# Kernel optimization log

Hardware: AMD Instinct MI355X
Metric: run time of the kernel (lower is better)

The kernel has to match this reference:

```python
import jax, jax.numpy as jnp
import numpy as np

NUM_HEADS = 16

def setup_inputs() -> dict:
    key = jax.random.key(0)
    k1, k2, k3, k4 = jax.random.split(key, 4)
    B, S, D = 4, 4096, 2048
    scale = 1.0 / np.sqrt(D)
    return {
        "x": jax.random.normal(k1, (B, S, D), dtype=jnp.float32),
        "W_q": jax.random.normal(k2, (D, D), dtype=jnp.float32) * scale,
        "W_kv": jax.random.normal(k3, (D, D), dtype=jnp.float32) * scale,
        "W_o": jax.random.normal(k4, (D, D), dtype=jnp.float32) * scale,
    }

def _l2_normalize_complex(z):
    # torch.norm(z, dim=-1, keepdim=True) for complex: sqrt(sum |z|^2)
    n = jnp.sqrt(jnp.sum(jnp.abs(z) ** 2, axis=-1, keepdims=True))
    return z / n

def reference(x, W_q, W_kv, W_o):
    B, S, D = x.shape
    H = NUM_HEADS
    hd = D // H
    # Linear (no bias), torch convention: x @ W.T
    q = (x @ W_q.T).reshape(B, S, H, hd)
    kv = (x @ W_kv.T).reshape(B, S, H, hd)
    # HRR binding: FFT along head dim
    qf = jnp.fft.fft(q, axis=-1)
    kvf = jnp.fft.fft(kv, axis=-1)
    qf = _l2_normalize_complex(qf)
    kvf = _l2_normalize_complex(kvf)
    # causal=True: cumulative sum of bound key-values over sequence
    kvf = jnp.cumsum(kvf, axis=1)
    qv = qf * kvf
    values_hat = jnp.fft.ifft(qv, axis=-1).real.astype(x.dtype)
    values_hat = values_hat.reshape(B, S, D)
    return values_hat @ W_o.T
```

## Files before the change

kernel.cpp:

```cpp
#include <hip/hip_runtime.h>
#include <hip/hip_bf16.h>


typedef unsigned short u16;
typedef unsigned int u32;
typedef __attribute__((ext_vector_type(8))) short short8;
typedef __attribute__((ext_vector_type(4))) float f32x4;

__device__ __forceinline__ float bf2f(u16 u) {
  u32 x = ((u32)u) << 16;
  float f; __builtin_memcpy(&f, &x, 4); return f;
}
__device__ __forceinline__ u16 f2bf(float f) {
  __hip_bfloat16 h = __float2bfloat16(f);
  u16 u; __builtin_memcpy(&u, &h, 2); return u;
}
__device__ __forceinline__ u32 pack2(float a, float b) {
  return (u32)f2bf(a) | ((u32)f2bf(b) << 16);
}

#define GLD16(gp, lp)                                                        \
  __builtin_amdgcn_global_load_lds(                                          \
      (const __attribute__((address_space(1))) void*)(gp),                   \
      (__attribute__((address_space(3))) void*)(lp), 16, 0, 0)

__device__ __forceinline__ unsigned ldsoff(const void* p) {
  return (unsigned)(size_t)(const __attribute__((address_space(3))) char*)p;
}

#define DSR(dst, ad, im)                                                     \
  asm volatile("ds_read_b128 %0, %1 offset:%c2"                              \
               : "=v"(dst) : "v"(ad), "i"(im))

#define MM2(ACCE, X0, X1, Y0, Y1)                                            \
  ACCE = __builtin_amdgcn_mfma_f32_16x16x32_bf16(X0, Y0, ACCE, 0, 0, 0);     \
  ACCE = __builtin_amdgcn_mfma_f32_16x16x32_bf16(X1, Y1, ACCE, 0, 0, 0)

template <int EPI>
__global__ __launch_bounds__(512, 2) void gemm256(
    const u16* __restrict__ A, const u16* __restrict__ B, void* __restrict__ C,
    int N, int K) {
  __shared__ alignas(1024) char smem[131072];
  const int NT = K >> 6;
  const int ntn = N >> 8;
  const int nwg = gridDim.x;
  int wg = blockIdx.x;
  wg = (wg & 7) * (nwg >> 3) + (wg >> 3);
  const int bm = wg / ntn, bn = wg % ntn;
  const long rowBase = (long)bm << 8, colBase = (long)bn << 8;

  const int tid = threadIdx.x;
  const int w = tid >> 6, lane = tid & 63;
  const int quad = lane >> 4, l16 = lane & 15;
  const int wm = w >> 2, wn = w & 3;

  const int grow = w * 8 + (lane >> 3);
  const int gcol = ((lane & 7) * 8) ^ ((lane >> 4) << 4);
  const long voff = (long)grow * K + gcol;
  const u16* Abase = A + rowBase * (long)K;
  const u16* Bbase = B + colBase * (long)K;
  char* ldsA = smem;
  char* ldsB = smem + 65536;

#define STG_A(v, h)                                                          \
  do {                                                                       \
    char* d_ = ldsA + (((v)&1) << 15) + ((h) << 14) + (w << 10);             \
    GLD16(Abase + ((h) * 128L) * K + (long)(v) * 64 + voff, d_);             \
    GLD16(Abase + ((h) * 128L + 64) * K + (long)(v) * 64 + voff, d_ + 8192); \
  } while (0)
#define STG_B(v, h)                                                          \
  do {                                                                       \
    char* d_ = ldsB + (((v)&1) << 15) + ((h) << 14) + (w << 10);             \
    GLD16(Bbase + ((h) * 128L) * K + (long)(v) * 64 + voff, d_);             \
    GLD16(Bbase + ((h) * 128L + 64) * K + (long)(v) * 64 + voff, d_ + 8192); \
  } while (0)

  const int cb0 = (quad << 4) ^ (((l16 >> 1) & 3) << 5);
  const unsigned bA0 = ldsoff(ldsA + (wm * 128 + l16) * 128) + cb0;
  const unsigned bA1 = bA0 ^ 64;
  const unsigned bB0 = ldsoff(ldsB + (wn * 64 + l16) * 128) + cb0;
  const unsigned bB1 = bB0 ^ 64;

  short8 aL[8], aH[8], bl[4], bh[4];
  f32x4 acc[8][4] = {};

  STG_A(0, 0); STG_A(0, 1); STG_B(0, 0); STG_B(0, 1);
  STG_B(1, 0); STG_B(1, 1);
  asm volatile("s_waitcnt vmcnt(4)");
  __builtin_amdgcn_s_barrier();

#define CLUSTER(BODY)                                                        \
  __builtin_amdgcn_sched_barrier(0);                                         \
  __builtin_amdgcn_s_setprio(1);                                             \
  BODY                                                                       \
  __builtin_amdgcn_s_setprio(0);                                             \
  __builtin_amdgcn_sched_barrier(0)

#define Q3P_BODY                                                             \
  _Pragma("unroll") for (int i = 0; i < 4; i++)                              \
    _Pragma("unroll") for (int j = 0; j < 2; j++) {                          \
      MM2(acc[i+4][j+2], aH[2*i], aH[2*i+1], bh[2*j], bh[2*j+1]);            \
    }
#define Q0_BODY                                                              \
  _Pragma("unroll") for (int i = 0; i < 4; i++)                              \
    _Pragma("unroll") for (int j = 0; j < 2; j++) {                          \
      MM2(acc[i][j], aL[2*i], aL[2*i+1], bl[2*j], bl[2*j+1]);                \
    }
#define Q1_BODY                                                              \
  _Pragma("unroll") for (int i = 0; i < 4; i++)                              \
    _Pragma("unroll") for (int j = 0; j < 2; j++) {                          \
      MM2(acc[i][j+2], aL[2*i], aL[2*i+1], bh[2*j], bh[2*j+1]);              \
    }
#define Q2_BODY                                                              \
  _Pragma("unroll") for (int i = 0; i < 4; i++)                              \
    _Pragma("unroll") for (int j = 0; j < 2; j++) {                          \
      MM2(acc[i+4][j], aH[2*i], aH[2*i+1], bl[2*j], bl[2*j+1]);              \
    }

#define RUN_TILE(uu, Q3P, SA_, SB_, WAITSTMT)                                \
  do {                                                                       \
    const unsigned bsel = ((uu) & 1) << 15;                                  \
    const unsigned aA0 = bA0 ^ bsel, aA1 = bA1 ^ bsel;                       \
    const unsigned aB0 = bB0 ^ bsel, aB1 = bB1 ^ bsel;                       \
                        \
    _Pragma("unroll") for (int i = 0; i < 4; i++) {                          \
      DSR(aL[2*i],   aA0, i * 2048);                                         \
      DSR(aL[2*i+1], aA1, i * 2048);                                         \
    }                                                                        \
    _Pragma("unroll") for (int j = 0; j < 2; j++) {                          \
      DSR(bl[2*j],   aB0, j * 2048);                                         \
      DSR(bl[2*j+1], aB1, j * 2048);                                         \
    }                                                                        \
    if (SA_) STG_A((uu) + 1, 0);                                             \
    __builtin_amdgcn_s_barrier();                                            \
    if (Q3P) { CLUSTER(Q3P_BODY); }                                          \
    __builtin_amdgcn_s_barrier();                                            \
      \
    _Pragma("unroll") for (int j = 0; j < 2; j++) {                          \
      DSR(bh[2*j],   aB0, (j + 2) * 2048);                                   \
      DSR(bh[2*j+1], aB1, (j + 2) * 2048);                                   \
    }                                                                        \
    if (SA_) STG_A((uu) + 1, 1);                                             \
    __builtin_amdgcn_s_barrier();                                            \
    asm volatile("s_waitcnt lgkmcnt(4)");                                    \
    CLUSTER(Q0_BODY);                                                        \
    __builtin_amdgcn_s_barrier();                                            \
         \
    _Pragma("unroll") for (int i = 0; i < 4; i++) {                          \
      DSR(aH[2*i],   aA0, (i + 4) * 2048);                                   \
      DSR(aH[2*i+1], aA1, (i + 4) * 2048);                                   \
    }                                                                        \
    if (SB_) STG_B((uu) + 2, 0);                                             \
    __builtin_amdgcn_s_barrier();                                            \
    asm volatile("s_waitcnt lgkmcnt(8)");                                    \
    CLUSTER(Q1_BODY);                                                        \
    __builtin_amdgcn_s_barrier();                                            \
        \
    if (SB_) STG_B((uu) + 2, 1);                                             \
    __builtin_amdgcn_s_barrier();                                            \
    asm volatile("s_waitcnt lgkmcnt(0)");                                    \
    CLUSTER(Q2_BODY);                                                        \
    WAITSTMT;                                                                \
    __builtin_amdgcn_s_barrier();                                            \
  } while (0)

  RUN_TILE(0, false, true, true, asm volatile("s_waitcnt vmcnt(4)"));
  for (int u = 1; u < NT - 2; ++u) {
    RUN_TILE(u, true, true, true, asm volatile("s_waitcnt vmcnt(4)"));
  }
  RUN_TILE(NT - 2, true, true, false, asm volatile("s_waitcnt vmcnt(0)"));
  RUN_TILE(NT - 1, true, false, false, (void)0);
  { Q3P_BODY }
#undef RUN_TILE
#undef Q3P_BODY
#undef Q0_BODY
#undef Q1_BODY
#undef Q2_BODY
#undef CLUSTER
#undef STG_A
#undef STG_B

  asm volatile("" ::: "memory");

  float scl[8][4];
#pragma unroll
  for (int i = 0; i < 8; i++)
#pragma unroll
    for (int r = 0; r < 4; r++) scl[i][r] = 1.0f;

  if (EPI == 2) {
    float* ssb = (float*)smem;
    __syncthreads();
#pragma unroll
    for (int i = 0; i < 8; i++)
#pragma unroll
      for (int r = 0; r < 4; r++) {
        float s = 0.f;
#pragma unroll
        for (int j = 0; j < 4; j++) { float v = acc[i][j][r]; s += v * v; }
        s += __shfl_xor(s, 1); s += __shfl_xor(s, 2);
        s += __shfl_xor(s, 4); s += __shfl_xor(s, 8);
        if (l16 == 0) ssb[((wm * 128 + i * 16 + quad * 4 + r) << 2) + wn] = s;
      }
    __syncthreads();
#pragma unroll
    for (int i = 0; i < 8; i++)
#pragma unroll
      for (int r = 0; r < 4; r++) {
        int row = wm * 128 + i * 16 + quad * 4 + r;
        float s = ssb[(row << 2) + (wn & 2)] + ssb[(row << 2) + (wn & 2) + 1];
        scl[i][r] = rsqrtf(128.0f * s);
      }
  }

#pragma unroll
  for (int i = 0; i < 8; i++) {
#pragma unroll
    for (int j = 0; j < 4; j++) {
      long row0 = rowBase + wm * 128 + i * 16 + quad * 4;
      long col = colBase + wn * 64 + j * 16 + l16;
#pragma unroll
      for (int r = 0; r < 4; r++) {
        float v = acc[i][j][r] * scl[i][r];
        long off = (row0 + r) * (long)N + col;
        if (EPI == 0) ((float*)C)[off] = v;
        else          ((u16*)C)[off] = f2bf(v);
      }
    }
  }
}

template <int EPI, bool FOLD>
__global__ __launch_bounds__(256, 2) void gemm_bt(
    const u16* __restrict__ A, const u16* __restrict__ B, void* __restrict__ C,
    int M, int N, int K, int lda) {
  const int ntiles = N >> 7;
  const int bid = blockIdx.x;
  const int bm = bid / ntiles, bn = bid % ntiles;
  const long rowBase = (long)bm * 128, colBase = (long)bn * 128;
  const long aOff = FOLD ? colBase : 0;
  const long bRowBase = FOLD ? 0 : colBase;

  __shared__ u16 As[128 * 32];
  __shared__ u16 Bs[128 * 32];
  __shared__ float ssbuf[128][2];

  const int tid = threadIdx.x;
  const int wave = tid >> 6, lane = tid & 63;
  const int quad = lane >> 4, l16 = lane & 15;
  const int waveRow = (wave >> 1) * 64, waveCol = (wave & 1) * 64;

  const int srow = lane >> 2, scol = (lane & 3) * 8;
  const u16* pa = A + (rowBase + wave * 32 + srow) * (long)lda + aOff + scol;
  const u16* pb = B + (bRowBase + wave * 32 + srow) * (long)K + scol;
  u16* lA0 = &As[(wave * 32) * 32];
  u16* lA1 = &As[(wave * 32 + 16) * 32];
  u16* lB0 = &Bs[(wave * 32) * 32];
  u16* lB1 = &Bs[(wave * 32 + 16) * 32];

  f32x4 acc[4][4] = {};

  for (int kt = 0; kt < K; kt += 32) {
    GLD16(pa + kt, lA0);
    GLD16(pa + kt + 16 * (long)lda, lA1);
    GLD16(pb + kt, lB0);
    GLD16(pb + kt + 16 * (long)K, lB1);
    __syncthreads();

    short8 af[4], bfr[4];
#pragma unroll
    for (int i = 0; i < 4; i++)
      af[i] = *(const short8*)&As[(waveRow + i * 16 + l16) * 32 + quad * 8];
#pragma unroll
    for (int j = 0; j < 4; j++)
      bfr[j] = *(const short8*)&Bs[(waveCol + j * 16 + l16) * 32 + quad * 8];
#pragma unroll
    for (int i = 0; i < 4; i++)
#pragma unroll
      for (int j = 0; j < 4; j++)
        acc[i][j] = __builtin_amdgcn_mfma_f32_16x16x32_bf16(af[i], bfr[j], acc[i][j], 0, 0, 0);
    __syncthreads();
  }

  float scl[4][4];
#pragma unroll
  for (int i = 0; i < 4; i++)
#pragma unroll
    for (int r = 0; r < 4; r++) scl[i][r] = 1.0f;

  if (EPI == 2) {
#pragma unroll
    for (int i = 0; i < 4; i++) {
#pragma unroll
      for (int r = 0; r < 4; r++) {
        float s = 0.f;
#pragma unroll
        for (int j = 0; j < 4; j++) { float v = acc[i][j][r]; s += v * v; }
#pragma unroll
        for (int m = 1; m < 16; m <<= 1) s += __shfl_xor(s, m);
        if (l16 == 0) ssbuf[waveRow + i * 16 + quad * 4 + r][wave & 1] = s;
      }
    }
    __syncthreads();
#pragma unroll
    for (int i = 0; i < 4; i++)
#pragma unroll
      for (int r = 0; r < 4; r++) {
        int row = waveRow + i * 16 + quad * 4 + r;
        scl[i][r] = rsqrtf(128.0f * (ssbuf[row][0] + ssbuf[row][1]));
      }
  }

#pragma unroll
  for (int i = 0; i < 4; i++) {
#pragma unroll
    for (int j = 0; j < 4; j++) {
      long row0 = rowBase + waveRow + i * 16 + quad * 4;
      long col = colBase + waveCol + j * 16 + l16;
#pragma unroll
      for (int r = 0; r < 4; r++) {
        float v = acc[i][j][r] * scl[i][r];
        long off = (row0 + r) * (long)N + col;
        if (EPI == 0) ((float*)C)[off] = v;
        else          ((u16*)C)[off] = f2bf(v);
      }
    }
  }
}

__global__ __launch_bounds__(256) void cast_f2b(const float* __restrict__ in,
                                                u16* __restrict__ out, int n4) {
  int i = blockIdx.x * 256 + threadIdx.x;
  if (i >= n4) return;
  float4 v = ((const float4*)in)[i];
  ushort4 u;
  u.x = f2bf(v.x); u.y = f2bf(v.y); u.z = f2bf(v.z); u.w = f2bf(v.w);
  ((ushort4*)out)[i] = u;
}

__global__ __launch_bounds__(256) void init_mats(u16* __restrict__ CSp,
                                                 u16* __restrict__ W2pT) {
  int idx = blockIdx.x * 256 + threadIdx.x;
  const float PI64 = 3.14159265358979323846f / 64.0f;
  if (idx < 16384) {
    int p = idx >> 7, n = idx & 127;
    int k = p >> 1;
    float v;
    if (p == 1) v = (n & 1) ? -1.f : 1.f;
    else {
      int t = (k * n) & 127;
      float ang = (float)t * PI64;
      v = (p & 1) ? -sinf(ang) : cosf(ang);
    }
    CSp[p * 128 + n] = f2bf(v);
  } else {
    int r = idx - 16384;
    int p = r >> 7, d = r & 127;
    int k = p >> 1;
    float v;
    if (p == 0) v = 1.0f / 128.0f;
    else if (p == 1) v = ((d & 1) ? -1.f : 1.f) / 128.0f;
    else {
      int t = (k * d) & 127;
      float ang = (float)t * PI64;
      v = ((p & 1) ? -2.f * sinf(ang) : 2.f * cosf(ang)) / 128.0f;
    }
    W2pT[p * 128 + d] = f2bf(v);
  }
}

__global__ __launch_bounds__(64) void scan_chunksum(const u16* __restrict__ F,
                                                    float* __restrict__ part) {
  int blk = blockIdx.x;
  int c = blk & 63, bh = blk >> 6;
  int h = bh & 15, b = bh >> 4;
  int l = threadIdx.x;
  float s0 = 0.f, s1 = 0.f;
  for (int t = c * 64; t < c * 64 + 64; ++t) {
    u32 u = ((const u32*)(F + ((long)(b * 4096 + t) * 32 + 16 + h) * 128))[l];
    s0 += bf2f((u16)(u & 0xffff));
    s1 += bf2f((u16)(u >> 16));
  }
  float2 w; w.x = s0; w.y = s1;
  ((float2*)part)[(long)blk * 64 + l] = w;
}

__global__ __launch_bounds__(128) void scan_exclusive(float* __restrict__ part) {
  int bh = blockIdx.x;
  int j = threadIdx.x;
  float run = 0.f;
  for (int c = 0; c < 64; ++c) {
    long idx = ((long)(bh * 64 + c)) * 128 + j;
    float v = part[idx];
    part[idx] = run;
    run += v;
  }
}

__global__ __launch_bounds__(64) void scan_main(const u16* __restrict__ F,
                                                u16* __restrict__ QV,
                                                const float* __restrict__ part) {
  int blk = blockIdx.x;
  int c = blk & 63, bh = blk >> 6;
  int h = bh & 15, b = bh >> 4;
  int l = threadIdx.x;
  float2 cc = ((const float2*)part)[(long)blk * 64 + l];
  float cr = cc.x, ci = cc.y;
  for (int t = c * 64; t < c * 64 + 64; ++t) {
    long m = (long)(b * 4096 + t);
    u32 ku = ((const u32*)(F + (m * 32 + 16 + h) * 128))[l];
    u32 qu = ((const u32*)(F + (m * 32 + h) * 128))[l];
    float kr = bf2f((u16)(ku & 0xffff)), ki = bf2f((u16)(ku >> 16));
    float qr = bf2f((u16)(qu & 0xffff)), qi = bf2f((u16)(qu >> 16));
    cr += kr; ci += ki;
    float vr, vi;
    if (l == 0) { vr = qr * cr; vi = qi * ci; }
    else { vr = qr * cr - qi * ci; vi = qr * ci + qi * cr; }
    ((u32*)(QV + (m * 16 + h) * 128))[l] = pack2(vr, vi);
  }
}

extern "C" void kernel_launch(void* const* d_in, const int* in_sizes, int n_in,
                              void* d_out, int out_size, void* d_ws, size_t ws_size,
                              hipStream_t stream) {
  const float* x   = (const float*)d_in[0];
  const float* Wq  = (const float*)d_in[1];
  const float* Wkv = (const float*)d_in[2];
  const float* Wo  = (const float*)d_in[3];
  float* out = (float*)d_out;

  const long M1 = 16384;
  const long D = 2048;
  const long R = M1 * 16;
  const long XE = M1 * D;
  const long WE = D * D;

  char* ws = (char*)d_ws;
  u16* qkh  = (u16*)(ws);
  u16* F    = (u16*)(ws + 134217728);
  u16* xb   = (u16*)(ws + 268435456);
  u16* wqkb = (u16*)(ws + 335544320);
  u16* wob  = (u16*)(ws + 352321536);
  u16* wo2  = (u16*)(ws + 360710144);
  u16* CSp  = (u16*)(ws + 369098752);
  u16* W2pT = (u16*)(ws + 369131520);
  float* part = (float*)(ws + 369164288);
  u16* QV = qkh;

  cast_f2b<<<(int)(XE / 4 / 256), 256, 0, stream>>>(x, xb, (int)(XE / 4));
  cast_f2b<<<(int)(WE / 4 / 256), 256, 0, stream>>>(Wq, wqkb, (int)(WE / 4));
  cast_f2b<<<(int)(WE / 4 / 256), 256, 0, stream>>>(Wkv, wqkb + WE, (int)(WE / 4));
  cast_f2b<<<(int)(WE / 4 / 256), 256, 0, stream>>>(Wo, wob, (int)(WE / 4));
  init_mats<<<128, 256, 0, stream>>>(CSp, W2pT);

  gemm_bt<1, true><<<16 * 16, 256, 0, stream>>>(wob, W2pT, wo2, 2048, 2048, 128, 2048);

  gemm256<2><<<(int)((M1 / 256) * (4096 / 256)), 512, 0, stream>>>(
      xb, wqkb, qkh, 4096, (int)D);

  gemm_bt<1, false><<<(int)(2 * R / 128), 256, 0, stream>>>(
      qkh, CSp, F, (int)(2 * R), 128, 128, 128);

  scan_chunksum<<<64 * 64, 64, 0, stream>>>(F, part);
  scan_exclusive<<<64, 128, 0, stream>>>(part);
  scan_main<<<64 * 64, 64, 0, stream>>>(F, QV, part);

  gemm256<0><<<(int)((M1 / 256) * (D / 256)), 512, 0, stream>>>(
      QV, wo2, out, (int)D, (int)D);
}
```

Baseline: 739.6 us.

## Restructure GEMM main loop to issue all LDS reads upfront with fewer barriers

```diff
diff --git a/kernel.cpp b/kernel.cpp
--- a/kernel.cpp
+++ b/kernel.cpp
@@ -88,19 +88,8 @@
   STG_B(1, 0); STG_B(1, 1);
   asm volatile("s_waitcnt vmcnt(4)");
   __builtin_amdgcn_s_barrier();
-
-#define CLUSTER(BODY)                                                        \
-  __builtin_amdgcn_sched_barrier(0);                                         \
-  __builtin_amdgcn_s_setprio(1);                                             \
-  BODY                                                                       \
-  __builtin_amdgcn_s_setprio(0);                                             \
-  __builtin_amdgcn_sched_barrier(0)
-
-#define Q3P_BODY                                                             \
-  _Pragma("unroll") for (int i = 0; i < 4; i++)                              \
-    _Pragma("unroll") for (int j = 0; j < 2; j++) {                          \
-      MM2(acc[i+4][j+2], aH[2*i], aH[2*i+1], bh[2*j], bh[2*j+1]);            \
-    }
+  __builtin_amdgcn_sched_barrier(0);
+
 #define Q0_BODY                                                              \
   _Pragma("unroll") for (int i = 0; i < 4; i++)                              \
     _Pragma("unroll") for (int j = 0; j < 2; j++) {                          \
@@ -116,13 +105,18 @@
     _Pragma("unroll") for (int j = 0; j < 2; j++) {                          \
       MM2(acc[i+4][j], aH[2*i], aH[2*i+1], bl[2*j], bl[2*j+1]);              \
     }
-
-#define RUN_TILE(uu, Q3P, SA_, SB_, WAITSTMT)                                \
+#define Q3_BODY                                                              \
+  _Pragma("unroll") for (int i = 0; i < 4; i++)                              \
+    _Pragma("unroll") for (int j = 0; j < 2; j++) {                          \
+      MM2(acc[i+4][j+2], aH[2*i], aH[2*i+1], bh[2*j], bh[2*j+1]);            \
+    }
+
+#define RUN_TILE(uu, SA_, SB_, WAITSTMT)                                     \
   do {                                                                       \
     const unsigned bsel = ((uu) & 1) << 15;                                  \
     const unsigned aA0 = bA0 ^ bsel, aA1 = bA1 ^ bsel;                       \
     const unsigned aB0 = bB0 ^ bsel, aB1 = bB1 ^ bsel;                       \
-                        \
+                   \
     _Pragma("unroll") for (int i = 0; i < 4; i++) {                          \
       DSR(aL[2*i],   aA0, i * 2048);                                         \
       DSR(aL[2*i+1], aA1, i * 2048);                                         \
@@ -131,52 +125,54 @@
       DSR(bl[2*j],   aB0, j * 2048);                                         \
       DSR(bl[2*j+1], aB1, j * 2048);                                         \
     }                                                                        \
-    if (SA_) STG_A((uu) + 1, 0);                                             \
-    __builtin_amdgcn_s_barrier();                                            \
-    if (Q3P) { CLUSTER(Q3P_BODY); }                                          \
-    __builtin_amdgcn_s_barrier();                                            \
-      \
     _Pragma("unroll") for (int j = 0; j < 2; j++) {                          \
       DSR(bh[2*j],   aB0, (j + 2) * 2048);                                   \
       DSR(bh[2*j+1], aB1, (j + 2) * 2048);                                   \
     }                                                                        \
-    if (SA_) STG_A((uu) + 1, 1);                                             \
-    __builtin_amdgcn_s_barrier();                                            \
-    asm volatile("s_waitcnt lgkmcnt(4)");                                    \
-    CLUSTER(Q0_BODY);                                                        \
-    __builtin_amdgcn_s_barrier();                                            \
-         \
     _Pragma("unroll") for (int i = 0; i < 4; i++) {                          \
       DSR(aH[2*i],   aA0, (i + 4) * 2048);                                   \
       DSR(aH[2*i+1], aA1, (i + 4) * 2048);                                   \
     }                                                                        \
-    if (SB_) STG_B((uu) + 2, 0);                                             \
+    if (SA_) { STG_A((uu) + 1, 0); STG_A((uu) + 1, 1); }                     \
+                       \
+    asm volatile("s_waitcnt lgkmcnt(12)");                                   \
+    __builtin_amdgcn_sched_barrier(0);                                       \
+    __builtin_amdgcn_s_setprio(1);                                           \
+    Q0_BODY                                                                  \
+    __builtin_amdgcn_s_setprio(0);                                           \
+                                   \
+    asm volatile("s_waitcnt lgkmcnt(8)");                                    \
+    __builtin_amdgcn_sched_barrier(0);                                       \
+    __builtin_amdgcn_s_setprio(1);                                           \
+    Q1_BODY                                                                  \
+    __builtin_amdgcn_s_setprio(0);                                           \
+    \
+                       \
     __builtin_amdgcn_s_barrier();                                            \
-    asm volatile("s_waitcnt lgkmcnt(8)");                                    \
-    CLUSTER(Q1_BODY);                                                        \
-    __builtin_amdgcn_s_barrier();                                            \
-        \
-    if (SB_) STG_B((uu) + 2, 1);                                             \
-    __builtin_amdgcn_s_barrier();                                            \
+    __builtin_amdgcn_sched_barrier(0);                                       \
+    if (SB_) { STG_B((uu) + 2, 0); STG_B((uu) + 2, 1); }                     \
+                                                          \
     asm volatile("s_waitcnt lgkmcnt(0)");                                    \
-    CLUSTER(Q2_BODY);                                                        \
+    __builtin_amdgcn_sched_barrier(0);                                       \
+    __builtin_amdgcn_s_setprio(1);                                           \
+    Q2_BODY                                                                  \
+    Q3_BODY                                                                  \
+    __builtin_amdgcn_s_setprio(0);                                           \
     WAITSTMT;                                                                \
     __builtin_amdgcn_s_barrier();                                            \
+    __builtin_amdgcn_sched_barrier(0);                                       \
   } while (0)
 
-  RUN_TILE(0, false, true, true, asm volatile("s_waitcnt vmcnt(4)"));
-  for (int u = 1; u < NT - 2; ++u) {
-    RUN_TILE(u, true, true, true, asm volatile("s_waitcnt vmcnt(4)"));
-  }
-  RUN_TILE(NT - 2, true, true, false, asm volatile("s_waitcnt vmcnt(0)"));
-  RUN_TILE(NT - 1, true, false, false, (void)0);
-  { Q3P_BODY }
+  for (int u = 0; u < NT - 2; ++u) {
+    RUN_TILE(u, true, true, asm volatile("s_waitcnt vmcnt(4)"));
+  }
+  RUN_TILE(NT - 2, true, false, asm volatile("s_waitcnt vmcnt(0)"));
+  RUN_TILE(NT - 1, false, false, (void)0);
 #undef RUN_TILE
-#undef Q3P_BODY
 #undef Q0_BODY
 #undef Q1_BODY
 #undef Q2_BODY
-#undef CLUSTER
+#undef Q3_BODY
 #undef STG_A
 #undef STG_B
 
```

New measurement: 724.4 us. 2.1% less time.
